# Kernel optimization log

Measured on AMD Instinct MI355X. Metric: run time of the kernel, lower is better.

## Reference

```python
import jax, jax.numpy as jnp
import numpy as np

GRID_SIZE = 8
POSITIVE_MARGIN = 1.0
NEGATIVE_MARGIN = 0.2
LAMBDA_D = 250.0
B, Hc, Wc, D = 4, 60, 60, 64


def warp_points(points, homographies):
    """points: [N,2] in (y,x); homographies: [B,3,3]. Returns [B,N,2] in (y,x)."""
    n = points.shape[0]
    xy1 = jnp.concatenate([points[:, ::-1], jnp.ones((n, 1), points.dtype)], axis=-1)  # (x,y,1)
    w = jnp.einsum('bij,nj->bni', homographies, xy1)  # [B,N,3]
    w = w[..., :2] / w[..., 2:3]
    return w[..., ::-1]  # back to (y,x)


def setup_inputs() -> dict:
    key = jax.random.key(0)
    k1, k2, k3 = jax.random.split(key, 3)
    descriptors = jax.random.normal(k1, (B, Hc, Wc, D), dtype=jnp.float32)
    warped_descriptors = jax.random.normal(k2, (B, Hc, Wc, D), dtype=jnp.float32)
    # near-identity homographies so warped cell centers remain close to the grid
    homographies = jnp.eye(3, dtype=jnp.float32)[None] + 0.001 * jax.random.normal(
        k3, (B, 3, 3), dtype=jnp.float32)
    valid_mask = jnp.ones((B, Hc * GRID_SIZE, Wc * GRID_SIZE), dtype=jnp.float32)
    return {"descriptors": descriptors, "warped_descriptors": warped_descriptors,
            "homographies": homographies, "valid_mask": valid_mask}


def reference(descriptors, warped_descriptors, homographies, valid_mask):
    b, hc, wc, d = descriptors.shape
    g = GRID_SIZE

    # cell-center coordinates (y, x) at full resolution
    yy, xx = jnp.meshgrid(jnp.arange(hc), jnp.arange(wc), indexing='ij')
    coord_cells = jnp.stack([yy, xx], axis=-1).astype(jnp.float32) * g + g // 2  # [Hc,Wc,2]

    warped_coord_cells = warp_points(coord_cells.reshape(-1, 2), homographies)  # [B,Hc*Wc,2]
    cc = coord_cells.reshape(1, 1, 1, hc, wc, 2)
    wcc = warped_coord_cells.reshape(b, hc, wc, 1, 1, 2)
    cell_distances = jnp.linalg.norm(cc - wcc, axis=-1)  # [B,Hc,Wc,Hc,Wc]
    s = (cell_distances <= g - 0.5).astype(descriptors.dtype)

    # broadcast dot-product score tensor [B,Hc,Wc,Hc,Wc]
    dot = jnp.einsum('bijd,bkld->bijkl', descriptors, warped_descriptors)

    positive_dist = jnp.maximum(0.0, POSITIVE_MARGIN - dot)
    negative_dist = jnp.maximum(0.0, dot - NEGATIVE_MARGIN)
    loss = LAMBDA_D * s * positive_dist + (1.0 - s) * negative_dist

    # space-to-depth + prod over the g*g block == per-cell AND of the valid mask
    vm = valid_mask.reshape(b, hc, g, wc, g)
    vm = jnp.prod(vm, axis=(2, 4))  # [B,Hc,Wc]
    vm = vm.reshape(b, 1, 1, hc, wc)

    normalization = jnp.sum(vm) * jnp.float32(hc * wc)
    return jnp.sum(vm * loss) / normalization
```

## Files before the change

kernel.cpp:

```cpp
#include <hip/hip_runtime.h>
#include <hip/hip_bf16.h>

#define HC 60
#define WCC 60
#define DD 64
#define NCELL (HC * WCC)
#define NBC (4 * NCELL)
#define IMG (HC * 8)
#define MPAD 3840
#define NT 15

#define CVT_BLOCKS 480
#define VM_BLOCKS 57
#define WC_BLOCKS 60
#define PREP_BLOCKS (CVT_BLOCKS + VM_BLOCKS + WC_BLOCKS)
#define GEMM_BLOCKS (NT * NT * 4)

typedef __bf16 bf16x8 __attribute__((ext_vector_type(8)));
typedef float f32x4 __attribute__((ext_vector_type(4)));
typedef unsigned short u16x8 __attribute__((ext_vector_type(8)));

__device__ inline unsigned short f2bf(float f) {
    union { float f; unsigned u; } x; x.f = f;
    unsigned u = x.u;
    unsigned r = (u + 0x7fffu + ((u >> 16) & 1u)) >> 16;
    return (unsigned short)r;
}

__device__ inline void gload_lds16(const void* g, void* l) {
    __builtin_amdgcn_global_load_lds(
        (const __attribute__((address_space(1))) unsigned int*)g,
        (__attribute__((address_space(3))) unsigned int*)l, 16, 0, 0);
}

__device__ inline int div60(int v) { return (v * 17477) >> 20; }

__global__ __launch_bounds__(256) void dl_prep_kernel(
    const float* __restrict__ desc, const float* __restrict__ wdesc,
    const float* __restrict__ homog, const float* __restrict__ mask,
    unsigned short* __restrict__ descb, unsigned short* __restrict__ wdescb,
    float* __restrict__ vm, float* __restrict__ vpart, float2* __restrict__ wcent)
{
    const int bid = blockIdx.x;
    const int tid = threadIdx.x;

    if (bid < CVT_BLOCKS) {
        int t = bid * 256 + tid;
        int brow = t >> 3;
        int col = (t & 7) * 8;
        int b = brow / MPAD;
        int row = brow - b * MPAD;
        u16x8 oa = (u16x8)0, ob = (u16x8)0;
        if (row < NCELL) {
            size_t src = ((size_t)(b * NCELL + row)) * DD + col;
            float4 a0 = *(const float4*)(desc + src);
            float4 a1 = *(const float4*)(desc + src + 4);
            float4 b0 = *(const float4*)(wdesc + src);
            float4 b1 = *(const float4*)(wdesc + src + 4);
            oa[0] = f2bf(a0.x); oa[1] = f2bf(a0.y); oa[2] = f2bf(a0.z); oa[3] = f2bf(a0.w);
            oa[4] = f2bf(a1.x); oa[5] = f2bf(a1.y); oa[6] = f2bf(a1.z); oa[7] = f2bf(a1.w);
            ob[0] = f2bf(b0.x); ob[1] = f2bf(b0.y); ob[2] = f2bf(b0.z); ob[3] = f2bf(b0.w);
            ob[4] = f2bf(b1.x); ob[5] = f2bf(b1.y); ob[6] = f2bf(b1.z); ob[7] = f2bf(b1.w);
        }
        size_t dst = (size_t)brow * DD + col;
        *(u16x8*)(descb + dst) = oa;
        *(u16x8*)(wdescb + dst) = ob;
    } else if (bid < CVT_BLOCKS + VM_BLOCKS) {
        int vb = bid - CVT_BLOCKS;
        int cell = vb * 256 + tid;
        float v = 0.f;
        if (cell < NBC) {
            int b = cell / NCELL;
            int rem = cell % NCELL;
            int k = rem / WCC, l = rem % WCC;
            const float* p = mask + (size_t)b * IMG * IMG + (size_t)(k * 8) * IMG + l * 8;
            float prod = 1.f;
#pragma unroll
            for (int dy = 0; dy < 8; ++dy) {
                float4 a0 = *(const float4*)(p + (size_t)dy * IMG);
                float4 a1 = *(const float4*)(p + (size_t)dy * IMG + 4);
                prod *= a0.x * a0.y * a0.z * a0.w * a1.x * a1.y * a1.z * a1.w;
            }
            vm[cell] = prod;
            v = prod;
        }
#pragma unroll
        for (int off = 32; off > 0; off >>= 1) v += __shfl_xor(v, off);
        __shared__ float sp[4];
        if ((tid & 63) == 0) sp[tid >> 6] = v;
        __syncthreads();
        if (tid == 0) vpart[vb] = sp[0] + sp[1] + sp[2] + sp[3];
    } else {
        int t = (bid - CVT_BLOCKS - VM_BLOCKS) * 256 + tid;
        int b = t / MPAD;
        int r = t - b * MPAD;
        float2 o;
        if (r < NCELL) {
            int i = div60(r);
            int j = r - i * WCC;
            const float* H = homog + b * 9;
            float x = (float)(j * 8 + 4), y = (float)(i * 8 + 4);
            float X2 = H[6] * x + H[7] * y + H[8];
            o.x = (H[3] * x + H[4] * y + H[5]) / X2;
            o.y = (H[0] * x + H[1] * y + H[2]) / X2;
        } else {
            o.x = 1e9f; o.y = 1e9f;
        }
        wcent[t] = o;
    }
}

__global__ __launch_bounds__(512, 2) void dl_gemm_loss_kernel(
    const unsigned short* __restrict__ descb, const unsigned short* __restrict__ wdescb,
    const float* __restrict__ vm, const float2* __restrict__ wcent,
    float* __restrict__ gpart)
{
    __shared__ unsigned char sA[256 * 128];
    __shared__ unsigned char sB[256 * 128];
    __shared__ float2 swcent[256];
    __shared__ float swave[8];

    const int b = blockIdx.z;
    const int m0 = blockIdx.x * 256;
    const int n0 = blockIdx.y * 256;
    const int tid = threadIdx.x;
    const int lane = tid & 63;
    const int wv = tid >> 6;

    const unsigned char* gA = (const unsigned char*)(descb + (size_t)b * MPAD * DD) + (size_t)m0 * 128;
    const unsigned char* gB = (const unsigned char*)(wdescb + (size_t)b * MPAD * DD) + (size_t)n0 * 128;

    {
        const int swz = ((lane & 7) ^ (lane >> 3)) << 4;
        const int lrow = lane >> 3;
#pragma unroll
        for (int t = 0; t < 4; ++t) {
            int row = wv * 32 + t * 8 + lrow;
            gload_lds16(gA + (size_t)row * 128 + swz, sA + wv * 4096 + t * 1024);
            gload_lds16(gB + (size_t)row * 128 + swz, sB + wv * 4096 + t * 1024);
        }
    }
    if (tid < 256) swcent[tid] = wcent[b * MPAD + m0 + tid];
    __syncthreads();

    const int wr = wv >> 2;
    const int wc = wv & 3;
    const int frow = lane & 15;
    const int kg = (lane >> 4) * 16;

    f32x4 acc[8][4];
#pragma unroll
    for (int i2 = 0; i2 < 8; ++i2)
#pragma unroll
        for (int j2 = 0; j2 < 4; ++j2)
            acc[i2][j2] = (f32x4)(0.f);

#pragma unroll
    for (int kk = 0; kk < 2; ++kk) {
        int kbyte = kk * 64 + kg;
        bf16x8 afr[8], bfr[4];
#pragma unroll
        for (int f = 0; f < 8; ++f) {
            int ra = wr * 128 + f * 16 + frow;
            afr[f] = *(const bf16x8*)(sA + ra * 128 + (kbyte ^ ((ra & 7) << 4)));
        }
#pragma unroll
        for (int f = 0; f < 4; ++f) {
            int rb = wc * 64 + f * 16 + frow;
            bfr[f] = *(const bf16x8*)(sB + rb * 128 + (kbyte ^ ((rb & 7) << 4)));
        }
#pragma unroll
        for (int fi = 0; fi < 8; ++fi)
#pragma unroll
            for (int fj = 0; fj < 4; ++fj)
                acc[fi][fj] = __builtin_amdgcn_mfma_f32_16x16x32_bf16(
                    afr[fi], bfr[fj], acc[fi][fj], 0, 0, 0);
    }

    float cyv[4], cxv[4], vmv[4];
#pragma unroll
    for (int fj = 0; fj < 4; ++fj) {
        int col = n0 + wc * 64 + fj * 16 + frow;
        int k = div60(col);
        int l = col - k * WCC;
        cyv[fj] = (float)(k * 8 + 4);
        cxv[fj] = (float)(l * 8 + 4);
        vmv[fj] = (col < NCELL) ? vm[b * NCELL + col] : 0.f;
    }

    float wlo = 1e30f, whi = -1e30f;
#pragma unroll
    for (int t = 0; t < 2; ++t) {
        float wyv = swcent[wr * 128 + t * 64 + lane].x;
        wlo = fminf(wlo, wyv); whi = fmaxf(whi, wyv);
    }
#pragma unroll
    for (int off = 32; off > 0; off >>= 1) {
        wlo = fminf(wlo, __shfl_xor(wlo, off));
        whi = fmaxf(whi, __shfl_xor(whi, off));
    }
    int c0 = n0 + wc * 64, c1 = c0 + 63;
    float cy0 = (float)(div60(c0) * 8 + 4) - 7.5f;
    float cy1 = (float)(div60(c1) * 8 + 4) + 7.5f;
    bool full = (whi >= cy0) && (wlo <= cy1);

    float partial = 0.f;
    if (full) {
#pragma unroll
        for (int fi = 0; fi < 8; ++fi) {
#pragma unroll
            for (int q = 0; q < 4; ++q) {
                float2 w2 = swcent[wr * 128 + fi * 16 + (lane >> 4) * 4 + q];
#pragma unroll
                for (int fj = 0; fj < 4; ++fj) {
                    float dot = acc[fi][fj][q];
                    float ddy = cyv[fj] - w2.x;
                    float ddx = cxv[fj] - w2.y;
                    float d2 = ddy * ddy + ddx * ddx;
                    float rn = fmaxf(dot - 0.2f, 0.f);
                    float rp = 250.f * fmaxf(1.f - dot, 0.f);
                    float sel = (d2 <= 56.25f) ? rp : rn;
                    partial += vmv[fj] * sel;
                }
            }
        }
    } else {
#pragma unroll
        for (int fi = 0; fi < 8; ++fi)
#pragma unroll
            for (int fj = 0; fj < 4; ++fj)
#pragma unroll
                for (int q = 0; q < 4; ++q)
                    partial += vmv[fj] * fmaxf(acc[fi][fj][q] - 0.2f, 0.f);
    }

#pragma unroll
    for (int off = 32; off > 0; off >>= 1) partial += __shfl_xor(partial, off);
    if (lane == 0) swave[wv] = partial;
    __syncthreads();
    if (tid == 0) {
        float s = 0.f;
#pragma unroll
        for (int w = 0; w < 8; ++w) s += swave[w];
        gpart[blockIdx.x + NT * (blockIdx.y + NT * b)] = s;
    }
}

__global__ __launch_bounds__(256) void dl_final_kernel(
    const float* __restrict__ vpart, const float* __restrict__ gpart,
    float* __restrict__ out)
{
    int tid = threadIdx.x;
    float ls = 0.f, vs = 0.f;
    for (int i = tid; i < GEMM_BLOCKS; i += 256) ls += gpart[i];
    for (int i = tid; i < VM_BLOCKS; i += 256) vs += vpart[i];
#pragma unroll
    for (int off = 32; off > 0; off >>= 1) {
        ls += __shfl_xor(ls, off);
        vs += __shfl_xor(vs, off);
    }
    __shared__ float sl[4], sv[4];
    if ((tid & 63) == 0) { sl[tid >> 6] = ls; sv[tid >> 6] = vs; }
    __syncthreads();
    if (tid == 0) {
        float L = sl[0] + sl[1] + sl[2] + sl[3];
        float V = sv[0] + sv[1] + sv[2] + sv[3];
        out[0] = L / (V * (float)NCELL);
    }
}

extern "C" void kernel_launch(void* const* d_in, const int* in_sizes, int n_in,
                              void* d_out, int out_size, void* d_ws, size_t ws_size,
                              hipStream_t stream) {
    const float* desc  = (const float*)d_in[0];
    const float* wdesc = (const float*)d_in[1];
    const float* homog = (const float*)d_in[2];
    const float* mask  = (const float*)d_in[3];
    float* out = (float*)d_out;
    float* wsf = (float*)d_ws;

    float* vpart = wsf;
    float* vm    = wsf + 64;
    float* gpart = wsf + 64 + NBC;
    float2* wcent = (float2*)(wsf + 15400);
    unsigned short* descb  = (unsigned short*)(wsf + 46208);
    unsigned short* wdescb = descb + (size_t)4 * MPAD * DD;

    hipLaunchKernelGGL(dl_prep_kernel, dim3(PREP_BLOCKS), dim3(256), 0, stream,
                       desc, wdesc, homog, mask, descb, wdescb, vm, vpart, wcent);
    hipLaunchKernelGGL(dl_gemm_loss_kernel, dim3(NT, NT, 4), dim3(512), 0, stream,
                       descb, wdescb, vm, wcent, gpart);
    hipLaunchKernelGGL(dl_final_kernel, dim3(1), dim3(256), 0, stream,
                       vpart, gpart, out);
}
```

Baseline: 39.16 us.

## Shrink GEMM-loss tiles to 128x128 with 256 threads and fold negative-margin offset

The fused GEMM+loss kernel moves from 256x256 tiles with 512 threads to 128x128 tiles with 256 threads. The grid grows from 900 to 3600 blocks, which spreads work over more CUs and lowers per-thread accumulator pressure. The loss rewrite computes max(dot,0.2) instead of max(dot-0.2,0) and subtracts the constant 0.2*MPAD*V once in the final kernel, removing a subtract per element. The wcent min/max range check is moved before the barrier to overlap with the async LDS loads. The costs are more partial sums to reduce, more redundant staging loads, and a global-constant correction that must match the padded column count exactly.

```diff
diff --git a/kernel.cpp b/kernel.cpp
--- a/kernel.cpp
+++ b/kernel.cpp
@@ -8,13 +8,13 @@
 #define NBC (4 * NCELL)
 #define IMG (HC * 8)
 #define MPAD 3840
-#define NT 15
+#define NT2 30
 
 #define CVT_BLOCKS 480
 #define VM_BLOCKS 57
 #define WC_BLOCKS 60
 #define PREP_BLOCKS (CVT_BLOCKS + VM_BLOCKS + WC_BLOCKS)
-#define GEMM_BLOCKS (NT * NT * 4)
+#define GEMM_BLOCKS (NT2 * NT2 * 4)
 
 typedef __bf16 bf16x8 __attribute__((ext_vector_type(8)));
 typedef float f32x4 __attribute__((ext_vector_type(4)));
@@ -110,19 +110,19 @@
     }
 }
 
-__global__ __launch_bounds__(512, 2) void dl_gemm_loss_kernel(
+__global__ __launch_bounds__(256, 3) void dl_gemm_loss_kernel(
     const unsigned short* __restrict__ descb, const unsigned short* __restrict__ wdescb,
     const float* __restrict__ vm, const float2* __restrict__ wcent,
     float* __restrict__ gpart)
 {
-    __shared__ unsigned char sA[256 * 128];
-    __shared__ unsigned char sB[256 * 128];
-    __shared__ float2 swcent[256];
-    __shared__ float swave[8];
+    __shared__ unsigned char sA[128 * 128];
+    __shared__ unsigned char sB[128 * 128];
+    __shared__ float2 swc[128];
+    __shared__ float swave[4];
 
     const int b = blockIdx.z;
-    const int m0 = blockIdx.x * 256;
-    const int n0 = blockIdx.y * 256;
+    const int m0 = blockIdx.x * 128;
+    const int n0 = blockIdx.y * 128;
     const int tid = threadIdx.x;
     const int lane = tid & 63;
     const int wv = tid >> 6;
@@ -140,42 +140,11 @@
             gload_lds16(gB + (size_t)row * 128 + swz, sB + wv * 4096 + t * 1024);
         }
     }
-    if (tid < 256) swcent[tid] = wcent[b * MPAD + m0 + tid];
-    __syncthreads();
-
-    const int wr = wv >> 2;
-    const int wc = wv & 3;
+    if (tid < 128) swc[tid] = wcent[b * MPAD + m0 + tid];
+
+    const int wr = wv >> 1, wc = wv & 1;
     const int frow = lane & 15;
     const int kg = (lane >> 4) * 16;
-
-    f32x4 acc[8][4];
-#pragma unroll
-    for (int i2 = 0; i2 < 8; ++i2)
-#pragma unroll
-        for (int j2 = 0; j2 < 4; ++j2)
-            acc[i2][j2] = (f32x4)(0.f);
-
-#pragma unroll
-    for (int kk = 0; kk < 2; ++kk) {
-        int kbyte = kk * 64 + kg;
-        bf16x8 afr[8], bfr[4];
-#pragma unroll
-        for (int f = 0; f < 8; ++f) {
-            int ra = wr * 128 + f * 16 + frow;
-            afr[f] = *(const bf16x8*)(sA + ra * 128 + (kbyte ^ ((ra & 7) << 4)));
-        }
-#pragma unroll
-        for (int f = 0; f < 4; ++f) {
-            int rb = wc * 64 + f * 16 + frow;
-            bfr[f] = *(const bf16x8*)(sB + rb * 128 + (kbyte ^ ((rb & 7) << 4)));
-        }
-#pragma unroll
-        for (int fi = 0; fi < 8; ++fi)
-#pragma unroll
-            for (int fj = 0; fj < 4; ++fj)
-                acc[fi][fj] = __builtin_amdgcn_mfma_f32_16x16x32_bf16(
-                    afr[fi], bfr[fj], acc[fi][fj], 0, 0, 0);
-    }
 
     float cyv[4], cxv[4], vmv[4];
 #pragma unroll
@@ -187,63 +156,85 @@
         cxv[fj] = (float)(l * 8 + 4);
         vmv[fj] = (col < NCELL) ? vm[b * NCELL + col] : 0.f;
     }
-
-    float wlo = 1e30f, whi = -1e30f;
-#pragma unroll
-    for (int t = 0; t < 2; ++t) {
-        float wyv = swcent[wr * 128 + t * 64 + lane].x;
-        wlo = fminf(wlo, wyv); whi = fmaxf(whi, wyv);
-    }
+    float wyl = wcent[b * MPAD + m0 + wr * 64 + lane].x;
+    float wlo = wyl, whi = wyl;
 #pragma unroll
     for (int off = 32; off > 0; off >>= 1) {
         wlo = fminf(wlo, __shfl_xor(wlo, off));
         whi = fmaxf(whi, __shfl_xor(whi, off));
     }
-    int c0 = n0 + wc * 64, c1 = c0 + 63;
+    int c0 = n0 + wc * 64;
     float cy0 = (float)(div60(c0) * 8 + 4) - 7.5f;
-    float cy1 = (float)(div60(c1) * 8 + 4) + 7.5f;
+    float cy1 = (float)(div60(c0 + 63) * 8 + 4) + 7.5f;
     bool full = (whi >= cy0) && (wlo <= cy1);
+
+    __syncthreads();
+
+    f32x4 acc[4][4];
+#pragma unroll
+    for (int i2 = 0; i2 < 4; ++i2)
+#pragma unroll
+        for (int j2 = 0; j2 < 4; ++j2)
+            acc[i2][j2] = (f32x4)(0.f);
+
+#pragma unroll
+    for (int kk = 0; kk < 2; ++kk) {
+        int kbyte = kk * 64 + kg;
+        bf16x8 afr[4], bfr[4];
+#pragma unroll
+        for (int f = 0; f < 4; ++f) {
+            int ra = wr * 64 + f * 16 + frow;
+            afr[f] = *(const bf16x8*)(sA + ra * 128 + (kbyte ^ ((ra & 7) << 4)));
+            int rb = wc * 64 + f * 16 + frow;
+            bfr[f] = *(const bf16x8*)(sB + rb * 128 + (kbyte ^ ((rb & 7) << 4)));
+        }
+#pragma unroll
+        for (int fi = 0; fi < 4; ++fi)
+#pragma unroll
+            for (int fj = 0; fj < 4; ++fj)
+                acc[fi][fj] = __builtin_amdgcn_mfma_f32_16x16x32_bf16(
+                    afr[fi], bfr[fj], acc[fi][fj], 0, 0, 0);
+    }
 
     float partial = 0.f;
     if (full) {
 #pragma unroll
-        for (int fi = 0; fi < 8; ++fi) {
+        for (int fi = 0; fi < 4; ++fi) {
 #pragma unroll
             for (int q = 0; q < 4; ++q) {
-                float2 w2 = swcent[wr * 128 + fi * 16 + (lane >> 4) * 4 + q];
+                float2 w2 = swc[wr * 64 + fi * 16 + (lane >> 4) * 4 + q];
 #pragma unroll
                 for (int fj = 0; fj < 4; ++fj) {
                     float dot = acc[fi][fj][q];
                     float ddy = cyv[fj] - w2.x;
                     float ddx = cxv[fj] - w2.y;
                     float d2 = ddy * ddy + ddx * ddx;
-                    float rn = fmaxf(dot - 0.2f, 0.f);
-                    float rp = 250.f * fmaxf(1.f - dot, 0.f);
-                    float sel = (d2 <= 56.25f) ? rp : rn;
-                    partial += vmv[fj] * sel;
+                    float pos = 250.f * fmaxf(1.f - dot, 0.f) + 0.2f;
+                    float neg = fmaxf(dot, 0.2f);
+                    partial += vmv[fj] * ((d2 <= 56.25f) ? pos : neg);
                 }
             }
         }
     } else {
 #pragma unroll
-        for (int fi = 0; fi < 8; ++fi)
-#pragma unroll
-            for (int fj = 0; fj < 4; ++fj)
+        for (int fj = 0; fj < 4; ++fj) {
+            float cs = 0.f;
+#pragma unroll
+            for (int fi = 0; fi < 4; ++fi)
 #pragma unroll
                 for (int q = 0; q < 4; ++q)
-                    partial += vmv[fj] * fmaxf(acc[fi][fj][q] - 0.2f, 0.f);
+                    cs += fmaxf(acc[fi][fj][q], 0.2f);
+            partial = fmaf(vmv[fj], cs, partial);
+        }
     }
 
 #pragma unroll
     for (int off = 32; off > 0; off >>= 1) partial += __shfl_xor(partial, off);
     if (lane == 0) swave[wv] = partial;
     __syncthreads();
-    if (tid == 0) {
-        float s = 0.f;
-#pragma unroll
-        for (int w = 0; w < 8; ++w) s += swave[w];
-        gpart[blockIdx.x + NT * (blockIdx.y + NT * b)] = s;
-    }
+    if (tid == 0)
+        gpart[blockIdx.x + NT2 * (blockIdx.y + NT2 * b)] =
+            swave[0] + swave[1] + swave[2] + swave[3];
 }
 
 __global__ __launch_bounds__(256) void dl_final_kernel(
@@ -265,6 +256,7 @@
     if (tid == 0) {
         float L = sl[0] + sl[1] + sl[2] + sl[3];
         float V = sv[0] + sv[1] + sv[2] + sv[3];
+        L -= 0.2f * (float)MPAD * V;
         out[0] = L / (V * (float)NCELL);
     }
 }
@@ -282,13 +274,13 @@
     float* vpart = wsf;
     float* vm    = wsf + 64;
     float* gpart = wsf + 64 + NBC;
-    float2* wcent = (float2*)(wsf + 15400);
-    unsigned short* descb  = (unsigned short*)(wsf + 46208);
+    float2* wcent = (float2*)(wsf + 18064);
+    unsigned short* descb  = (unsigned short*)(wsf + 49408);
     unsigned short* wdescb = descb + (size_t)4 * MPAD * DD;
 
     hipLaunchKernelGGL(dl_prep_kernel, dim3(PREP_BLOCKS), dim3(256), 0, stream,
                        desc, wdesc, homog, mask, descb, wdescb, vm, vpart, wcent);
-    hipLaunchKernelGGL(dl_gemm_loss_kernel, dim3(NT, NT, 4), dim3(512), 0, stream,
+    hipLaunchKernelGGL(dl_gemm_loss_kernel, dim3(NT2, NT2, 4), dim3(256), 0, stream,
                        descb, wdescb, vm, wcent, gpart);
     hipLaunchKernelGGL(dl_final_kernel, dim3(1), dim3(256), 0, stream,
                        vpart, gpart, out);
```

Result: faster. 36.71 us (-6.3%).
